# Optimization experiments

Hardware: AMD Instinct MI355X
Metric: run time of the kernel (lower is better)

## Reference

```python
import jax, jax.numpy as jnp
import numpy as np

EPS = 1e-12

def l2_normalize(x, axis=-1):
    # matches torch F.normalize(p=2, dim=1, eps=1e-12) for 2D input
    n = jnp.sqrt(jnp.sum(x * x, axis=axis, keepdims=True))
    return x / jnp.maximum(n, EPS)

def setup_inputs() -> dict:
    key = jax.random.key(0)
    ks = jax.random.split(key, 7)
    N, D = 8192, 256
    s = 1.0 / np.sqrt(D)
    x = jax.random.normal(ks[0], (N, D), dtype=jnp.float32)
    Wq = jax.random.uniform(ks[1], (D, D), jnp.float32, -s, s)
    bq = jax.random.uniform(ks[2], (D,), jnp.float32, -s, s)
    Wk = jax.random.uniform(ks[3], (D, D), jnp.float32, -s, s)
    bk = jax.random.uniform(ks[4], (D,), jnp.float32, -s, s)
    Wv = jax.random.uniform(ks[5], (D, D), jnp.float32, -s, s)
    bv = jax.random.uniform(ks[6], (D,), jnp.float32, -s, s)
    return {"x": x, "Wq": Wq, "bq": bq, "Wk": Wk, "bk": bk, "Wv": Wv, "bv": bv}

def reference(x, Wq, bq, Wk, bk, Wv, bv):
    q = l2_normalize(x @ Wq.T + bq)           # [N, D]
    k = l2_normalize(x @ Wk.T + bk)           # [N, D]
    v = x @ Wv.T + bv                         # [N, D]
    cos_sim = q @ k.T                         # [N, N]
    w = jax.nn.relu(cos_sim)
    # zero diagonal, then renormalize rows to sum 1
    N = w.shape[0]
    w = jnp.where(jnp.eye(N, dtype=bool), 0.0, w)
    w = w / jnp.maximum(jnp.sum(w, axis=-1, keepdims=True), EPS)
    return w @ v + x
```

## Files before the change

kernel.cpp:

```cpp
#include <hip/hip_runtime.h>

#define NROWS 8192
#define DDIM  256
#define KSPLIT 4
#define BM 128
#define BK 64
#define NT (NROWS / KSPLIT / BK)

typedef __bf16 bf16x8 __attribute__((ext_vector_type(8)));
typedef float  f32x4  __attribute__((ext_vector_type(4)));

typedef __attribute__((address_space(1))) unsigned int uint_gas;
typedef __attribute__((address_space(3))) unsigned int uint_las;

__device__ __forceinline__ void gload_lds16(const void* g, void* l) {
  __builtin_amdgcn_global_load_lds((const uint_gas*)g, (uint_las*)l, 16, 0, 0);
}

__device__ __forceinline__ unsigned int f2bf_bits(float f) {
  union { float f; unsigned int u; } v; v.f = f;
  unsigned int r = v.u + 0x7FFFu + ((v.u >> 16) & 1u);
  return r >> 16;
}
__device__ __forceinline__ float bf2f(unsigned int b) {
  union { unsigned int u; float f; } v; v.u = b << 16;
  return v.f;
}
__device__ __forceinline__ unsigned int pack2bf(float a, float b) {
  union { unsigned int u; __bf16 h[2]; } p;
  p.h[0] = (__bf16)a; p.h[1] = (__bf16)b;
  return p.u;
}

__global__ __launch_bounds__(256) void convert_kernel(
    const float* __restrict__ wq, const float* __restrict__ wk,
    const float* __restrict__ wv, unsigned short* __restrict__ Wb)
{
  int i = blockIdx.x * 256 + threadIdx.x;
  const int nw4 = DDIM * DDIM / 4;
  const float4* src; int j;
  if (i < nw4)          { src = (const float4*)wq; j = i; }
  else if (i < 2*nw4)   { src = (const float4*)wk; j = i - nw4; }
  else                  { src = (const float4*)wv; j = i - 2*nw4; }
  float4 f = src[j];
  ushort4 o;
  o.x = (unsigned short)f2bf_bits(f.x);
  o.y = (unsigned short)f2bf_bits(f.y);
  o.z = (unsigned short)f2bf_bits(f.z);
  o.w = (unsigned short)f2bf_bits(f.w);
  ((ushort4*)(Wb))[i] = o;
}

__global__ __launch_bounds__(256) void qkv_kernel(
    const float* __restrict__ bq, const float* __restrict__ bk, const float* __restrict__ bv,
    const float* __restrict__ x, const unsigned short* __restrict__ Wb,
    unsigned short* __restrict__ qb, unsigned short* __restrict__ kb,
    unsigned short* __restrict__ vb, unsigned short* __restrict__ vT)
{
  __shared__ unsigned short vstage[DDIM * 72];
  const int t = threadIdx.x;
  const int w = t >> 6, l = t & 63;
  const int c = l & 15, g = l >> 4;
  const int out = blockIdx.x / 128;
  const int mb  = blockIdx.x % 128;
  const int row0 = mb * 64;
  const int rw = row0 + w * 16;

  bf16x8 a[8];
  #pragma unroll
  for (int ks = 0; ks < 8; ks++) {
    const float* p = x + (size_t)(rw + c) * DDIM + ks * 32 + g * 8;
    float4 f0 = *(const float4*)p;
    float4 f1 = *(const float4*)(p + 4);
    union { bf16x8 v; unsigned short s[8]; } u;
    u.s[0] = (unsigned short)f2bf_bits(f0.x);
    u.s[1] = (unsigned short)f2bf_bits(f0.y);
    u.s[2] = (unsigned short)f2bf_bits(f0.z);
    u.s[3] = (unsigned short)f2bf_bits(f0.w);
    u.s[4] = (unsigned short)f2bf_bits(f1.x);
    u.s[5] = (unsigned short)f2bf_bits(f1.y);
    u.s[6] = (unsigned short)f2bf_bits(f1.z);
    u.s[7] = (unsigned short)f2bf_bits(f1.w);
    a[ks] = u.v;
  }

  const unsigned short* W = Wb + out * DDIM * DDIM;
  const float* bias = (out == 0) ? bq : (out == 1) ? bk : bv;
  unsigned short* dst = (out == 0) ? qb : (out == 1) ? kb : vb;
  f32x4 vals[16];
  #pragma unroll
  for (int ct = 0; ct < 16; ct++) {
    f32x4 acc = {0.f, 0.f, 0.f, 0.f};
    #pragma unroll
    for (int ks = 0; ks < 8; ks++) {
      bf16x8 b = *(const bf16x8*)(W + (size_t)(ct * 16 + c) * DDIM + ks * 32 + g * 8);
      acc = __builtin_amdgcn_mfma_f32_16x16x32_bf16(a[ks], b, acc, 0, 0, 0);
    }
    float bias_v = bias[ct * 16 + c];
    #pragma unroll
    for (int r = 0; r < 4; r++) acc[r] += bias_v;
    vals[ct] = acc;
  }
  if (out < 2) {
    #pragma unroll
    for (int r = 0; r < 4; r++) {
      float ss = 0.f;
      #pragma unroll
      for (int ct = 0; ct < 16; ct++) ss += vals[ct][r] * vals[ct][r];
      ss += __shfl_xor(ss, 1); ss += __shfl_xor(ss, 2);
      ss += __shfl_xor(ss, 4); ss += __shfl_xor(ss, 8);
      float inv = 1.f / fmaxf(sqrtf(ss), 1e-12f);
      #pragma unroll
      for (int ct = 0; ct < 16; ct++) vals[ct][r] *= inv;
    }
  }
  #pragma unroll
  for (int ct = 0; ct < 16; ct++) {
    #pragma unroll
    for (int r = 0; r < 4; r++) {
      unsigned int bits = f2bf_bits(vals[ct][r]);
      unsigned int ob = (unsigned int)__shfl_xor((int)bits, 1);
      if (!(l & 1))
        *(unsigned int*)(dst + (size_t)(rw + g * 4 + r) * DDIM + ct * 16 + c) =
            bits | (ob << 16);
      if (out == 2)
        vstage[(ct * 16 + c) * 72 + (w * 16 + g * 4 + r)] = (unsigned short)bits;
    }
  }
  if (out == 2) {
    __syncthreads();
    #pragma unroll
    for (int p = 0; p < 8; p++) {
      int dd = (t >> 3) + p * 32;
      int ch = t & 7;
      *(uint4*)(vT + (size_t)dd * NROWS + row0 + ch * 8) =
          *(const uint4*)(vstage + dd * 72 + ch * 8);
    }
  }
}

__global__ __launch_bounds__(512, 2) void attn_kernel(
    const unsigned short* __restrict__ qb, const unsigned short* __restrict__ kb,
    const unsigned short* __restrict__ vT,
    float* __restrict__ nump, float* __restrict__ denp)
{
  __shared__ __align__(16) char smem[147456];
  char* kbuf = smem;
  char* vbuf = smem + 65536;
  char* P    = smem + 131072;

  const int t = threadIdx.x;
  const int w = t >> 6, l = t & 63;
  const int c = l & 15, g = l >> 4;
  const int wr = w >> 1, wc = w & 1;
  const int bid = blockIdx.x;
  const int split = bid & (KSPLIT - 1);
  const int mb = bid >> 2;
  const int q0 = mb * BM;
  const int kbase0 = split * (NROWS / KSPLIT);

  const char* kbc = (const char*)kb;
  const char* vtc = (const char*)vT;

  bf16x8 qa[2][8];
  #pragma unroll
  for (int rt = 0; rt < 2; rt++)
    #pragma unroll
    for (int ks = 0; ks < 8; ks++)
      qa[rt][ks] = *(const bf16x8*)(qb + (size_t)(q0 + wr*32 + rt*16 + c) * DDIM + ks*32 + g*8);

  f32x4 oacc[2][8];
  #pragma unroll
  for (int rt = 0; rt < 2; rt++)
    #pragma unroll
    for (int dt = 0; dt < 8; dt++)
      oacc[rt][dt] = (f32x4){0.f, 0.f, 0.f, 0.f};
  float denl[2] = {0.f, 0.f};

  auto stage = [&](int buf, int it) {
    const int kbase = kbase0 + it * BK;
    const char* ksrc = kbc + (size_t)kbase * 512;
    #pragma unroll
    for (int i = 0; i < 4; i++) {
      int n = i * 512 + t;
      int row = n >> 5, slot = n & 31;
      gload_lds16(ksrc + row * 512 + ((slot ^ (row & 7)) * 16),
                  kbuf + buf * 32768 + i * 8192 + w * 1024);
    }
    const char* vsrc = vtc + (size_t)kbase * 2;
    #pragma unroll
    for (int i = 0; i < 4; i++) {
      int n = i * 512 + t;
      int dd = n >> 3, slot = n & 7;
      gload_lds16(vsrc + (size_t)dd * (NROWS * 2) + ((slot ^ (dd & 7)) * 16),
                  vbuf + buf * 32768 + i * 8192 + w * 1024);
    }
  };

  stage(0, 0);
  asm volatile("s_waitcnt vmcnt(0)" ::: "memory");
  __builtin_amdgcn_sched_barrier(0);
  __builtin_amdgcn_s_barrier();
  __builtin_amdgcn_sched_barrier(0);

  for (int it = 0; it < NT; ++it) {
    const int cur = it & 1;
    if (it + 1 < NT) stage(cur ^ 1, it + 1);
    __builtin_amdgcn_sched_barrier(0);

    const char* kcur = kbuf + cur * 32768;
    f32x4 sacc[2][2];
    #pragma unroll
    for (int kt = 0; kt < 2; kt++)
      #pragma unroll
      for (int rt = 0; rt < 2; rt++)
        sacc[kt][rt] = (f32x4){0.f, 0.f, 0.f, 0.f};
    #pragma unroll
    for (int ks = 0; ks < 8; ks++) {
      bf16x8 kf[2];
      #pragma unroll
      for (int kt = 0; kt < 2; kt++) {
        int rl = wc * 32 + kt * 16 + c;
        kf[kt] = *(const bf16x8*)(kcur + rl * 512 + ((ks * 64 + g * 16) ^ ((rl & 7) << 4)));
      }
      #pragma unroll
      for (int kt = 0; kt < 2; kt++)
        #pragma unroll
        for (int rt = 0; rt < 2; rt++)
          sacc[kt][rt] = __builtin_amdgcn_mfma_f32_16x16x32_bf16(kf[kt], qa[rt][ks],
                                                                 sacc[kt][rt], 0, 0, 0);
    }
    #pragma unroll
    for (int kt = 0; kt < 2; kt++)
      #pragma unroll
      for (int rt = 0; rt < 2; rt++) {
        float v0 = fmaxf(sacc[kt][rt][0], 0.f);
        float v1 = fmaxf(sacc[kt][rt][1], 0.f);
        float v2 = fmaxf(sacc[kt][rt][2], 0.f);
        float v3 = fmaxf(sacc[kt][rt][3], 0.f);
        denl[rt] += (v0 + v1) + (v2 + v3);
        uint2 d2;
        d2.x = pack2bf(v0, v1);
        d2.y = pack2bf(v2, v3);
        int prow = wr * 32 + rt * 16 + c;
        int pcol = wc * 32 + kt * 16 + g * 4;
        *(uint2*)(P + prow * 128 + ((pcol * 2) ^ ((prow & 7) << 4))) = d2;
      }
    asm volatile("s_waitcnt lgkmcnt(0)" ::: "memory");
    __builtin_amdgcn_sched_barrier(0);
    __builtin_amdgcn_s_barrier();
    __builtin_amdgcn_sched_barrier(0);

    const char* vcur = vbuf + cur * 32768;
    #pragma unroll
    for (int ks2 = 0; ks2 < 2; ks2++) {
      bf16x8 pa[2];
      #pragma unroll
      for (int rt = 0; rt < 2; rt++) {
        int prow = wr * 32 + rt * 16 + c;
        pa[rt] = *(const bf16x8*)(P + prow * 128 +
                                  ((ks2 * 64 + g * 16) ^ ((prow & 7) << 4)));
      }
      #pragma unroll
      for (int dt = 0; dt < 8; dt++) {
        int dl = wc * 128 + dt * 16 + c;
        bf16x8 vf = *(const bf16x8*)(vcur + dl * 128 +
                                     ((ks2 * 64 + g * 16) ^ ((dl & 7) << 4)));
        #pragma unroll
        for (int rt = 0; rt < 2; rt++)
          oacc[rt][dt] = __builtin_amdgcn_mfma_f32_16x16x32_bf16(pa[rt], vf,
                                                                 oacc[rt][dt], 0, 0, 0);
      }
    }
    asm volatile("s_waitcnt vmcnt(0)" ::: "memory");
    __builtin_amdgcn_sched_barrier(0);
    __builtin_amdgcn_s_barrier();
    __builtin_amdgcn_sched_barrier(0);
  }

  float* np = nump + (size_t)split * NROWS * DDIM;
  #pragma unroll
  for (int rt = 0; rt < 2; rt++)
    #pragma unroll
    for (int dt = 0; dt < 8; dt++)
      #pragma unroll
      for (int r = 0; r < 4; r++) {
        int rowg = q0 + wr*32 + rt*16 + g*4 + r;
        int col  = wc*128 + dt*16 + c;
        np[(size_t)rowg * DDIM + col] = oacc[rt][dt][r];
      }
  #pragma unroll
  for (int rt = 0; rt < 2; rt++) {
    float d = denl[rt];
    d += __shfl_xor(d, 16);
    d += __shfl_xor(d, 32);
    if (l < 16)
      denp[((size_t)split * 2 + wc) * NROWS + q0 + wr*32 + rt*16 + l] = d;
  }
}

__global__ __launch_bounds__(256) void combine_kernel(
    const float* __restrict__ x, const unsigned short* __restrict__ qb,
    const unsigned short* __restrict__ kb, const unsigned short* __restrict__ vb,
    const float* __restrict__ nump, const float* __restrict__ denp,
    float* __restrict__ out)
{
  const int t = threadIdx.x;
  const int w = t >> 6, l = t & 63;
  const int i = blockIdx.x * 4 + w;

  ushort4 q4 = *(const ushort4*)(qb + (size_t)i * DDIM + l * 4);
  ushort4 k4 = *(const ushort4*)(kb + (size_t)i * DDIM + l * 4);
  float s = bf2f(q4.x) * bf2f(k4.x) + bf2f(q4.y) * bf2f(k4.y)
          + bf2f(q4.z) * bf2f(k4.z) + bf2f(q4.w) * bf2f(k4.w);
  #pragma unroll
  for (int m = 1; m < 64; m <<= 1) s += __shfl_xor(s, m);
  float r  = fmaxf(s, 0.f);
  float rb = bf2f(f2bf_bits(r));

  float den = 0.f;
  #pragma unroll
  for (int sp = 0; sp < KSPLIT * 2; sp++)
    den += denp[(size_t)sp * NROWS + i];
  float inv = 1.f / fmaxf(den - rb, 1e-12f);

  const int d0 = l * 4;
  float4 acc = *(const float4*)(nump + (size_t)i * DDIM + d0);
  #pragma unroll
  for (int sp = 1; sp < KSPLIT; sp++) {
    float4 a2 = *(const float4*)(nump + (size_t)sp * NROWS * DDIM + (size_t)i * DDIM + d0);
    acc.x += a2.x; acc.y += a2.y; acc.z += a2.z; acc.w += a2.w;
  }
  ushort4 v4 = *(const ushort4*)(vb + (size_t)i * DDIM + d0);
  float4 xx = *(const float4*)(x + (size_t)i * DDIM + d0);
  float4 o;
  o.x = (acc.x - rb * bf2f(v4.x)) * inv + xx.x;
  o.y = (acc.y - rb * bf2f(v4.y)) * inv + xx.y;
  o.z = (acc.z - rb * bf2f(v4.z)) * inv + xx.z;
  o.w = (acc.w - rb * bf2f(v4.w)) * inv + xx.w;
  *(float4*)(out + (size_t)i * DDIM + d0) = o;
}

extern "C" void kernel_launch(void* const* d_in, const int* in_sizes, int n_in,
                              void* d_out, int out_size, void* d_ws, size_t ws_size,
                              hipStream_t stream)
{
  const float* x  = (const float*)d_in[0];
  const float* Wq = (const float*)d_in[1];
  const float* bq = (const float*)d_in[2];
  const float* Wk = (const float*)d_in[3];
  const float* bk = (const float*)d_in[4];
  const float* Wv = (const float*)d_in[5];
  const float* bv = (const float*)d_in[6];

  char* ws = (char*)d_ws;
  unsigned short* Wb  = (unsigned short*)(ws + 0);
  unsigned short* qb  = (unsigned short*)(ws + 393216);
  unsigned short* kb  = (unsigned short*)(ws + 4587520);
  unsigned short* vb  = (unsigned short*)(ws + 8781824);
  unsigned short* vT  = (unsigned short*)(ws + 12976128);
  float* nump = (float*)(ws + 17170432);
  float* denp = (float*)(ws + 50724864);

  convert_kernel<<<192, 256, 0, stream>>>(Wq, Wk, Wv, Wb);
  qkv_kernel<<<384, 256, 0, stream>>>(bq, bk, bv, x, Wb, qb, kb, vb, vT);
  attn_kernel<<<(NROWS / BM) * KSPLIT, 512, 0, stream>>>(qb, kb, vT, nump, denp);
  combine_kernel<<<NROWS / 4, 256, 0, stream>>>(x, qb, kb, vb, nump, denp, (float*)d_out);
}
```

Measured before the change: 132.3 us.

## Switch attention matmuls to 32x32x16 MFMA with new wave tiling

Replaces the 16x16x32 bf16 MFMA tiles with 32x32x16 MFMA in both the QK^T score stage and the P·V accumulation stage. It reorganizes wave ownership: a 4x2 wave grid for scores and a 2x4 wave grid for the output, with new swizzled LDS addressing for the P and V fragments. The aim is fewer LDS fragment loads per FLOP and fewer MFMA issues, since the larger tile has higher operand reuse. In exchange it changes the register layout of the accumulators and the output store pattern, and register pressure could rise.

```diff
diff --git a/kernel.cpp b/kernel.cpp
--- a/kernel.cpp
+++ b/kernel.cpp
@@ -9,6 +9,7 @@
 
 typedef __bf16 bf16x8 __attribute__((ext_vector_type(8)));
 typedef float  f32x4  __attribute__((ext_vector_type(4)));
+typedef float  f32x16 __attribute__((ext_vector_type(16)));
 
 typedef __attribute__((address_space(1))) unsigned int uint_gas;
 typedef __attribute__((address_space(3))) unsigned int uint_las;
@@ -151,8 +152,9 @@
 
   const int t = threadIdx.x;
   const int w = t >> 6, l = t & 63;
-  const int c = l & 15, g = l >> 4;
-  const int wr = w >> 1, wc = w & 1;
+  const int l31 = l & 31, hi = l >> 5;
+  const int sr = w >> 1, sc = w & 1;
+  const int pr = w >> 2, pc = w & 3;
   const int bid = blockIdx.x;
   const int split = bid & (KSPLIT - 1);
   const int mb = bid >> 2;
@@ -162,20 +164,21 @@
   const char* kbc = (const char*)kb;
   const char* vtc = (const char*)vT;
 
-  bf16x8 qa[2][8];
+  bf16x8 qa[16];
+  {
+    const unsigned short* qrowp = qb + (size_t)(q0 + sr * 32 + l31) * DDIM + hi * 8;
+    #pragma unroll
+    for (int m = 0; m < 16; m++)
+      qa[m] = *(const bf16x8*)(qrowp + m * 16);
+  }
+
+  f32x16 oacc[2][2];
   #pragma unroll
   for (int rt = 0; rt < 2; rt++)
     #pragma unroll
-    for (int ks = 0; ks < 8; ks++)
-      qa[rt][ks] = *(const bf16x8*)(qb + (size_t)(q0 + wr*32 + rt*16 + c) * DDIM + ks*32 + g*8);
-
-  f32x4 oacc[2][8];
-  #pragma unroll
-  for (int rt = 0; rt < 2; rt++)
-    #pragma unroll
-    for (int dt = 0; dt < 8; dt++)
-      oacc[rt][dt] = (f32x4){0.f, 0.f, 0.f, 0.f};
-  float denl[2] = {0.f, 0.f};
+    for (int dt = 0; dt < 2; dt++)
+      oacc[rt][dt] = (f32x16){0.f};
+  float denl = 0.f;
 
   auto stage = [&](int buf, int it) {
     const int kbase = kbase0 + it * BK;
@@ -209,43 +212,30 @@
     __builtin_amdgcn_sched_barrier(0);
 
     const char* kcur = kbuf + cur * 32768;
-    f32x4 sacc[2][2];
-    #pragma unroll
-    for (int kt = 0; kt < 2; kt++)
-      #pragma unroll
-      for (int rt = 0; rt < 2; rt++)
-        sacc[kt][rt] = (f32x4){0.f, 0.f, 0.f, 0.f};
-    #pragma unroll
-    for (int ks = 0; ks < 8; ks++) {
-      bf16x8 kf[2];
-      #pragma unroll
-      for (int kt = 0; kt < 2; kt++) {
-        int rl = wc * 32 + kt * 16 + c;
-        kf[kt] = *(const bf16x8*)(kcur + rl * 512 + ((ks * 64 + g * 16) ^ ((rl & 7) << 4)));
-      }
-      #pragma unroll
-      for (int kt = 0; kt < 2; kt++)
-        #pragma unroll
-        for (int rt = 0; rt < 2; rt++)
-          sacc[kt][rt] = __builtin_amdgcn_mfma_f32_16x16x32_bf16(kf[kt], qa[rt][ks],
-                                                                 sacc[kt][rt], 0, 0, 0);
-    }
-    #pragma unroll
-    for (int kt = 0; kt < 2; kt++)
-      #pragma unroll
-      for (int rt = 0; rt < 2; rt++) {
-        float v0 = fmaxf(sacc[kt][rt][0], 0.f);
-        float v1 = fmaxf(sacc[kt][rt][1], 0.f);
-        float v2 = fmaxf(sacc[kt][rt][2], 0.f);
-        float v3 = fmaxf(sacc[kt][rt][3], 0.f);
-        denl[rt] += (v0 + v1) + (v2 + v3);
+    const int krl = sc * 32 + l31;
+    f32x16 sacc = {0.f};
+    #pragma unroll
+    for (int m = 0; m < 16; m++) {
+      bf16x8 kf = *(const bf16x8*)(kcur + krl * 512 + ((m * 32 + hi * 16) ^ ((krl & 7) << 4)));
+      sacc = __builtin_amdgcn_mfma_f32_32x32x16_bf16(kf, qa[m], sacc, 0, 0, 0);
+    }
+    {
+      const int qrow = sr * 32 + l31;
+      char* prow = P + qrow * 128;
+      const int swz = (qrow & 7) << 4;
+      #pragma unroll
+      for (int j = 0; j < 4; j++) {
+        float v0 = fmaxf(sacc[4 * j + 0], 0.f);
+        float v1 = fmaxf(sacc[4 * j + 1], 0.f);
+        float v2 = fmaxf(sacc[4 * j + 2], 0.f);
+        float v3 = fmaxf(sacc[4 * j + 3], 0.f);
+        denl += (v0 + v1) + (v2 + v3);
         uint2 d2;
         d2.x = pack2bf(v0, v1);
         d2.y = pack2bf(v2, v3);
-        int prow = wr * 32 + rt * 16 + c;
-        int pcol = wc * 32 + kt * 16 + g * 4;
-        *(uint2*)(P + prow * 128 + ((pcol * 2) ^ ((prow & 7) << 4))) = d2;
+        *(uint2*)(prow + ((sc * 64 + j * 16 + hi * 8) ^ swz)) = d2;
       }
+    }
     asm volatile("s_waitcnt lgkmcnt(0)" ::: "memory");
     __builtin_amdgcn_sched_barrier(0);
     __builtin_amdgcn_s_barrier();
@@ -253,24 +243,26 @@
 
     const char* vcur = vbuf + cur * 32768;
     #pragma unroll
-    for (int ks2 = 0; ks2 < 2; ks2++) {
-      bf16x8 pa[2];
+    for (int ch = 0; ch < 4; ch++) {
+      bf16x8 pa[2], vf[2];
       #pragma unroll
       for (int rt = 0; rt < 2; rt++) {
-        int prow = wr * 32 + rt * 16 + c;
-        pa[rt] = *(const bf16x8*)(P + prow * 128 +
-                                  ((ks2 * 64 + g * 16) ^ ((prow & 7) << 4)));
+        int qrow = pr * 64 + rt * 32 + l31;
+        pa[rt] = *(const bf16x8*)(P + qrow * 128 +
+                                  ((ch * 32 + hi * 16) ^ ((qrow & 7) << 4)));
       }
       #pragma unroll
-      for (int dt = 0; dt < 8; dt++) {
-        int dl = wc * 128 + dt * 16 + c;
-        bf16x8 vf = *(const bf16x8*)(vcur + dl * 128 +
-                                     ((ks2 * 64 + g * 16) ^ ((dl & 7) << 4)));
+      for (int dt = 0; dt < 2; dt++) {
+        int dl = pc * 64 + dt * 32 + l31;
+        vf[dt] = *(const bf16x8*)(vcur + dl * 128 +
+                                  ((ch * 32 + hi * 16) ^ ((dl & 7) << 4)));
+      }
+      #pragma unroll
+      for (int rt = 0; rt < 2; rt++)
         #pragma unroll
-        for (int rt = 0; rt < 2; rt++)
-          oacc[rt][dt] = __builtin_amdgcn_mfma_f32_16x16x32_bf16(pa[rt], vf,
+        for (int dt = 0; dt < 2; dt++)
+          oacc[rt][dt] = __builtin_amdgcn_mfma_f32_32x32x16_bf16(pa[rt], vf[dt],
                                                                  oacc[rt][dt], 0, 0, 0);
-      }
     }
     asm volatile("s_waitcnt vmcnt(0)" ::: "memory");
     __builtin_amdgcn_sched_barrier(0);
@@ -282,20 +274,18 @@
   #pragma unroll
   for (int rt = 0; rt < 2; rt++)
     #pragma unroll
-    for (int dt = 0; dt < 8; dt++)
-      #pragma unroll
-      for (int r = 0; r < 4; r++) {
-        int rowg = q0 + wr*32 + rt*16 + g*4 + r;
-        int col  = wc*128 + dt*16 + c;
+    for (int dt = 0; dt < 2; dt++)
+      #pragma unroll
+      for (int r = 0; r < 16; r++) {
+        int rowg = q0 + pr * 64 + rt * 32 + (r & 3) + 8 * (r >> 2) + 4 * hi;
+        int col  = pc * 64 + dt * 32 + l31;
         np[(size_t)rowg * DDIM + col] = oacc[rt][dt][r];
       }
-  #pragma unroll
-  for (int rt = 0; rt < 2; rt++) {
-    float d = denl[rt];
-    d += __shfl_xor(d, 16);
+  {
+    float d = denl;
     d += __shfl_xor(d, 32);
-    if (l < 16)
-      denp[((size_t)split * 2 + wc) * NROWS + q0 + wr*32 + rt*16 + l] = d;
+    if (l < 32)
+      denp[((size_t)split * 2 + sc) * NROWS + q0 + sr * 32 + l] = d;
   }
 }
 
```

After: 132.1 us. About the same (-0.2%).
